# Performance work log

Measured on AMD Instinct MI355X. Metric: run time of the kernel, lower is better.

## Reference

```python
import jax, jax.numpy as jnp
import numpy as np

D_MODEL = 1024
H = 16
D_HEAD = D_MODEL // H
EPS = 1e-5  # torch LayerNorm default


def setup_inputs() -> dict:
    key = jax.random.key(0)
    ks = jax.random.split(key, 10)
    bs, seq = 4, 2048
    scale = 1.0 / np.sqrt(D_MODEL)
    return {
        "q": jax.random.normal(ks[0], (bs, seq, D_MODEL), jnp.float32),
        "k": jax.random.normal(ks[1], (bs, seq, D_MODEL), jnp.float32),
        "v": jax.random.normal(ks[2], (bs, seq, D_MODEL), jnp.float32),
        "zero_mask": jnp.zeros((bs, 1, 1, seq), jnp.float32),
        "Wq": jax.random.normal(ks[3], (D_MODEL, D_MODEL), jnp.float32) * scale,
        "Wk": jax.random.normal(ks[4], (D_MODEL, D_MODEL), jnp.float32) * scale,
        "Wv": jax.random.normal(ks[5], (D_MODEL, D_MODEL), jnp.float32) * scale,
        "Wo": jax.random.normal(ks[6], (D_MODEL, D_MODEL), jnp.float32) * scale,
        "gamma": jnp.ones((D_MODEL,), jnp.float32),
        "beta": jnp.zeros((D_MODEL,), jnp.float32),
    }


def reference(q, k, v, zero_mask, Wq, Wk, Wv, Wo, gamma, beta):
    bs, seq_q, _ = q.shape
    seq_k = k.shape[1]
    residual = q
    # Projections (torch Linear: x @ W.T), split into heads -> (bs, h, seq, d)
    qh = (q @ Wq.T).reshape(bs, seq_q, H, D_HEAD).transpose(0, 2, 1, 3)
    kh = (k @ Wk.T).reshape(bs, seq_k, H, D_HEAD).transpose(0, 2, 1, 3)
    vh = (v @ Wv.T).reshape(bs, seq_k, H, D_HEAD).transpose(0, 2, 1, 3)
    # Scaled dot-product attention with additive -1e9 * zero_mask
    att = jnp.einsum("bhqd,bhkd->bhqk", qh, kh) / np.sqrt(D_HEAD)
    att = att + zero_mask * -1e9
    att = jax.nn.softmax(att, axis=-1)
    # dropout: identity in eval-mode reference
    ctx = jnp.einsum("bhqk,bhkd->bhqd", att, vh)
    ctx = ctx.transpose(0, 2, 1, 3).reshape(bs, seq_q, D_MODEL)
    out = ctx @ Wo.T
    out = out + residual
    # LayerNorm over last dim
    mu = jnp.mean(out, axis=-1, keepdims=True)
    var = jnp.var(out, axis=-1, keepdims=True)
    out = (out - mu) * jax.lax.rsqrt(var + EPS) * gamma + beta
    return out
```

## Files before the change

kernel.cpp:

```cpp
#include <hip/hip_runtime.h>

typedef __bf16 bf16x8 __attribute__((ext_vector_type(8)));
typedef float  f32x4  __attribute__((ext_vector_type(4)));
typedef short  s16x4  __attribute__((ext_vector_type(4)));

#define D_MODEL 1024
#define SEQ 2048
#define BS 4
#define NH 16
#define DH 64
#define MTOT (BS * SEQ)

#define AS1 __attribute__((address_space(1)))
#define AS3 __attribute__((address_space(3)))

template <typename T>
__device__ inline bf16x8 ld8(const T* p);

template <>
__device__ inline bf16x8 ld8<float>(const float* p) {
    f32x4 a = *(const f32x4*)p;
    f32x4 b = *(const f32x4*)(p + 4);
    bf16x8 r;
    r[0] = (__bf16)a[0]; r[1] = (__bf16)a[1]; r[2] = (__bf16)a[2]; r[3] = (__bf16)a[3];
    r[4] = (__bf16)b[0]; r[5] = (__bf16)b[1]; r[6] = (__bf16)b[2]; r[7] = (__bf16)b[3];
    return r;
}

template <>
__device__ inline bf16x8 ld8<__bf16>(const __bf16* p) {
    return *(const bf16x8*)p;
}

__global__ __launch_bounds__(256) void cvt3_kernel(
    const float* __restrict__ a, const float* __restrict__ b, const float* __restrict__ c,
    __bf16* __restrict__ x, __bf16* __restrict__ y, __bf16* __restrict__ z)
{
    const float* s = (blockIdx.y == 0) ? a : (blockIdx.y == 1) ? b : c;
    __bf16*      d = (blockIdx.y == 0) ? x : (blockIdx.y == 1) ? y : z;
    const long i = ((long)blockIdx.x * 256 + threadIdx.x) * 8;
    *(bf16x8*)(d + i) = ld8<float>(s + i);
}

__global__ __launch_bounds__(256) void cvt4_kernel(
    const float* __restrict__ a, const float* __restrict__ b,
    const float* __restrict__ c, const float* __restrict__ e,
    __bf16* __restrict__ x, __bf16* __restrict__ y,
    __bf16* __restrict__ z, __bf16* __restrict__ w)
{
    const float* s = (blockIdx.y == 0) ? a : (blockIdx.y == 1) ? b : (blockIdx.y == 2) ? c : e;
    __bf16*      d = (blockIdx.y == 0) ? x : (blockIdx.y == 1) ? y : (blockIdx.y == 2) ? z : w;
    const long i = ((long)blockIdx.x * 256 + threadIdx.x) * 8;
    *(bf16x8*)(d + i) = ld8<float>(s + i);
}

__global__ __launch_bounds__(256) void gemm_bb(
    const __bf16* __restrict__ A, const __bf16* __restrict__ B,
    __bf16* __restrict__ C, int M, int N, int K)
{
    __shared__ __align__(16) __bf16 As[128 * 32];
    __shared__ __align__(16) __bf16 Bs[128 * 32];
    const int t = threadIdx.x;
    const int wave = t >> 6, lane = t & 63;
    const int quad = lane >> 4, l15 = lane & 15;
    const int wm = (wave >> 1) * 64, wn = (wave & 1) * 64;
    const long m0 = (long)blockIdx.x * 128;
    const long n0 = (long)blockIdx.y * 128;

    const __bf16* gA = A + (m0 + (t >> 2)) * (long)K + (t & 3) * 8;
    const __bf16* gB = B + (n0 + (t >> 2)) * (long)K + (t & 3) * 8;
    __bf16* lA0 = As + wave * 512;
    __bf16* lA1 = As + 2048 + wave * 512;
    __bf16* lB0 = Bs + wave * 512;
    __bf16* lB1 = Bs + 2048 + wave * 512;

    f32x4 acc[4][4] = {};

    for (int k0 = 0; k0 < K; k0 += 32) {
        __builtin_amdgcn_global_load_lds((const AS1 void*)(gA + k0),          (AS3 void*)lA0, 16, 0, 0);
        __builtin_amdgcn_global_load_lds((const AS1 void*)(gA + 64 * K + k0), (AS3 void*)lA1, 16, 0, 0);
        __builtin_amdgcn_global_load_lds((const AS1 void*)(gB + k0),          (AS3 void*)lB0, 16, 0, 0);
        __builtin_amdgcn_global_load_lds((const AS1 void*)(gB + 64 * K + k0), (AS3 void*)lB1, 16, 0, 0);
        __syncthreads();
        bf16x8 af[4], bfr[4];
#pragma unroll
        for (int i = 0; i < 4; ++i) af[i]  = *(const bf16x8*)&As[(wm + i * 16 + l15) * 32 + quad * 8];
#pragma unroll
        for (int i = 0; i < 4; ++i) bfr[i] = *(const bf16x8*)&Bs[(wn + i * 16 + l15) * 32 + quad * 8];
#pragma unroll
        for (int i = 0; i < 4; ++i)
#pragma unroll
            for (int j = 0; j < 4; ++j)
                acc[i][j] = __builtin_amdgcn_mfma_f32_16x16x32_bf16(af[i], bfr[j], acc[i][j], 0, 0, 0);
        __syncthreads();
    }

#pragma unroll
    for (int i = 0; i < 4; ++i)
#pragma unroll
        for (int j = 0; j < 4; ++j) {
            const long r = m0 + wm + i * 16 + quad * 4;
            const long c = n0 + wn + j * 16 + l15;
#pragma unroll
            for (int reg = 0; reg < 4; ++reg)
                C[(r + reg) * N + c] = (__bf16)acc[i][j][reg];
        }
}

template <typename TA, typename TB>
__global__ __launch_bounds__(256) void gemm_bt(
    const TA* __restrict__ A, const TB* __restrict__ B,
    __bf16* __restrict__ C, int M, int N, int K)
{
    __shared__ __align__(16) __bf16 As[128][48];
    __shared__ __align__(16) __bf16 Bs[128][48];
    const int t = threadIdx.x;
    const int wave = t >> 6, lane = t & 63;
    const int quad = lane >> 4, l15 = lane & 15;
    const int wm = (wave >> 1) * 64, wn = (wave & 1) * 64;
    const long m0 = (long)blockIdx.x * 128;
    const long n0 = (long)blockIdx.y * 128;
    const int sr = t >> 2;
    const int sc = (t & 3) * 8;

    f32x4 acc[4][4] = {};

    for (int k0 = 0; k0 < K; k0 += 32) {
        *(bf16x8*)&As[sr][sc]      = ld8<TA>(&A[(m0 + sr) * K + k0 + sc]);
        *(bf16x8*)&As[sr + 64][sc] = ld8<TA>(&A[(m0 + sr + 64) * K + k0 + sc]);
        *(bf16x8*)&Bs[sr][sc]      = ld8<TB>(&B[(n0 + sr) * K + k0 + sc]);
        *(bf16x8*)&Bs[sr + 64][sc] = ld8<TB>(&B[(n0 + sr + 64) * K + k0 + sc]);
        __syncthreads();
        bf16x8 af[4], bfr[4];
#pragma unroll
        for (int i = 0; i < 4; ++i) af[i]  = *(const bf16x8*)&As[wm + i * 16 + l15][quad * 8];
#pragma unroll
        for (int i = 0; i < 4; ++i) bfr[i] = *(const bf16x8*)&Bs[wn + i * 16 + l15][quad * 8];
#pragma unroll
        for (int i = 0; i < 4; ++i)
#pragma unroll
            for (int j = 0; j < 4; ++j)
                acc[i][j] = __builtin_amdgcn_mfma_f32_16x16x32_bf16(af[i], bfr[j], acc[i][j], 0, 0, 0);
        __syncthreads();
    }

#pragma unroll
    for (int i = 0; i < 4; ++i)
#pragma unroll
        for (int j = 0; j < 4; ++j) {
            const long r = m0 + wm + i * 16 + quad * 4;
            const long c = n0 + wn + j * 16 + l15;
#pragma unroll
            for (int reg = 0; reg < 4; ++reg)
                C[(r + reg) * N + c] = (__bf16)acc[i][j][reg];
        }
}

__global__ __launch_bounds__(256) void attn_kernel(
    const __bf16* Qp, const __bf16* __restrict__ Kp, const __bf16* __restrict__ Vp,
    const float* __restrict__ mask, __bf16* Ctx)
{
    __shared__ __align__(16) __bf16 Ks[64][72];
    __shared__ __align__(16) __bf16 Vt[64][76];
    __shared__ __align__(16) float  Ms[64];

    const int t = threadIdx.x;
    const int wave = t >> 6, lane = t & 63;
    const int quad = lane >> 4, l15 = lane & 15;
    const int qt = blockIdx.x;
    const int bh = blockIdx.y;
    const int b = bh >> 4, h = bh & 15;
    const long rowbase = (long)b * SEQ;
    const int q0 = qt * 128 + wave * 16;

    bf16x8 aq[2][2];
#pragma unroll
    for (int qi = 0; qi < 2; ++qi) {
        const long qrow = rowbase + q0 + qi * 64 + l15;
        const __bf16* qptr = Qp + qrow * D_MODEL + h * DH + quad * 8;
        aq[qi][0] = *(const bf16x8*)(qptr);
        aq[qi][1] = *(const bf16x8*)(qptr + 32);
    }

    float l_acc[2] = {0.f, 0.f};
    f32x4 acc_o[2][4] = {};

    const int sr = t >> 2, sc = (t & 3) * 16;
    const int kp2 = (t >> 3) * 2, dc = (t & 7) * 8;

    for (int kt = 0; kt < SEQ / 64; ++kt) {
        __syncthreads();
        {
            const __bf16* kptr = Kp + (rowbase + kt * 64 + sr) * D_MODEL + h * DH + sc;
            *(bf16x8*)&Ks[sr][sc]     = *(const bf16x8*)(kptr);
            *(bf16x8*)&Ks[sr][sc + 8] = *(const bf16x8*)(kptr + 8);
            const __bf16* vptr = Vp + (rowbase + kt * 64 + kp2) * D_MODEL + h * DH + dc;
            bf16x8 v0 = *(const bf16x8*)(vptr);
            bf16x8 v1 = *(const bf16x8*)(vptr + D_MODEL);
#pragma unroll
            for (int e = 0; e < 8; ++e) {
                union { __bf16 h2[2]; unsigned u; } pk;
                pk.h2[0] = v0[e]; pk.h2[1] = v1[e];
                *(unsigned*)&Vt[dc + e][kp2] = pk.u;
            }
            if (t < 64) Ms[t] = mask[(long)b * SEQ + kt * 64 + t] * -1e9f;
        }
        __syncthreads();

        bf16x8 kf[4][2];
#pragma unroll
        for (int nt = 0; nt < 4; ++nt)
#pragma unroll
            for (int ks = 0; ks < 2; ++ks)
                kf[nt][ks] = *(const bf16x8*)&Ks[nt * 16 + l15][ks * 32 + quad * 8];
        s16x4 vtf[4][4];
#pragma unroll
        for (int nt = 0; nt < 4; ++nt)
#pragma unroll
            for (int dt = 0; dt < 4; ++dt)
                vtf[nt][dt] = *(const s16x4*)&Vt[dt * 16 + l15][nt * 16 + quad * 4];
        f32x4 mv[4];
#pragma unroll
        for (int nt = 0; nt < 4; ++nt)
            mv[nt] = *(const f32x4*)&Ms[nt * 16 + quad * 4];

#pragma unroll
        for (int qi = 0; qi < 2; ++qi) {
            f32x4 st[4] = {};
#pragma unroll
            for (int ks = 0; ks < 2; ++ks)
#pragma unroll
                for (int nt = 0; nt < 4; ++nt)
                    st[nt] = __builtin_amdgcn_mfma_f32_16x16x32_bf16(kf[nt][ks], aq[qi][ks], st[nt], 0, 0, 0);
            s16x4 pp[4];
#pragma unroll
            for (int nt = 0; nt < 4; ++nt) {
                union { __bf16 hh[4]; s16x4 s; } u;
#pragma unroll
                for (int reg = 0; reg < 4; ++reg) {
                    const float pv = __expf(fmaf(st[nt][reg], 0.125f, mv[nt][reg]));
                    l_acc[qi] += pv;
                    u.hh[reg] = (__bf16)pv;
                }
                pp[nt] = u.s;
            }
#pragma unroll
            for (int nt = 0; nt < 4; ++nt)
#pragma unroll
                for (int dt = 0; dt < 4; ++dt)
                    acc_o[qi][dt] = __builtin_amdgcn_mfma_f32_16x16x16bf16_1k(pp[nt], vtf[nt][dt], acc_o[qi][dt], 0, 0, 0);
        }
    }

#pragma unroll
    for (int qi = 0; qi < 2; ++qi) {
        float l = l_acc[qi];
        l += __shfl_xor(l, 16, 64);
        l += __shfl_xor(l, 32, 64);
        const float inv = 1.f / l;
        float invq[4];
#pragma unroll
        for (int reg = 0; reg < 4; ++reg)
            invq[reg] = __shfl(inv, quad * 4 + reg, 64);
#pragma unroll
        for (int dt = 0; dt < 4; ++dt)
#pragma unroll
            for (int reg = 0; reg < 4; ++reg) {
                const long row = rowbase + q0 + qi * 64 + quad * 4 + reg;
                Ctx[row * D_MODEL + h * DH + dt * 16 + l15] = (__bf16)(acc_o[qi][dt][reg] * invq[reg]);
            }
    }
}

__global__ __launch_bounds__(256) void ln_kernel(
    const __bf16* __restrict__ Y, const float* __restrict__ R,
    const float* __restrict__ gamma, const float* __restrict__ beta,
    float* __restrict__ Out)
{
    __shared__ float red[8];
    const long row = blockIdx.x;
    const int t = threadIdx.x;
    const int wave = t >> 6, lane = t & 63;
    float x[4];
    float s = 0.f, s2 = 0.f;
#pragma unroll
    for (int i = 0; i < 4; ++i) {
        const int idx = i * 256 + t;
        const float v = (float)Y[row * D_MODEL + idx] + R[row * D_MODEL + idx];
        x[i] = v; s += v; s2 += v * v;
    }
#pragma unroll
    for (int off = 32; off >= 1; off >>= 1) {
        s  += __shfl_xor(s, off, 64);
        s2 += __shfl_xor(s2, off, 64);
    }
    if (lane == 0) { red[wave] = s; red[4 + wave] = s2; }
    __syncthreads();
    s  = red[0] + red[1] + red[2] + red[3];
    s2 = red[4] + red[5] + red[6] + red[7];
    const float mu   = s * (1.f / 1024.f);
    const float var  = s2 * (1.f / 1024.f) - mu * mu;
    const float rstd = rsqrtf(var + 1e-5f);
#pragma unroll
    for (int i = 0; i < 4; ++i) {
        const int idx = i * 256 + t;
        Out[row * D_MODEL + idx] = (x[i] - mu) * rstd * gamma[idx] + beta[idx];
    }
}

extern "C" void kernel_launch(void* const* d_in, const int* in_sizes, int n_in,
                              void* d_out, int out_size, void* d_ws, size_t ws_size,
                              hipStream_t stream)
{
    const float* q     = (const float*)d_in[0];
    const float* k     = (const float*)d_in[1];
    const float* v     = (const float*)d_in[2];
    const float* mask  = (const float*)d_in[3];
    const float* Wq    = (const float*)d_in[4];
    const float* Wk    = (const float*)d_in[5];
    const float* Wv    = (const float*)d_in[6];
    const float* Wo    = (const float*)d_in[7];
    const float* gamma = (const float*)d_in[8];
    const float* beta  = (const float*)d_in[9];
    float* out = (float*)d_out;

    const long NACT = (long)MTOT * D_MODEL;
    const long NW   = (long)D_MODEL * D_MODEL;
    dim3 gg(MTOT / 128, D_MODEL / 128);
    dim3 ga(SEQ / 128, BS * NH);

    if (ws_size >= (size_t)NACT * 2 * 4) {
        __bf16* qb = (__bf16*)d_ws;
        __bf16* kb = qb + NACT;
        __bf16* vb = kb + NACT;
        __bf16* Kp = vb + NACT;
        __bf16* Vp = (__bf16*)d_out;
        __bf16* Wb = Vp + NACT;
        __bf16 *Wqb = Wb, *Wkb = Wb + NW, *Wvb = Wb + 2 * NW, *Wob = Wb + 3 * NW;
        __bf16* Qp = kb;
        __bf16* Y  = qb;

        cvt3_kernel<<<dim3(NACT / 2048, 3), 256, 0, stream>>>(q, k, v, qb, kb, vb);
        cvt4_kernel<<<dim3(NW / 2048, 4), 256, 0, stream>>>(Wq, Wk, Wv, Wo, Wqb, Wkb, Wvb, Wob);

        gemm_bb<<<gg, 256, 0, stream>>>(kb, Wkb, Kp, MTOT, D_MODEL, D_MODEL);
        gemm_bb<<<gg, 256, 0, stream>>>(qb, Wqb, Qp, MTOT, D_MODEL, D_MODEL);
        gemm_bb<<<gg, 256, 0, stream>>>(vb, Wvb, Vp, MTOT, D_MODEL, D_MODEL);

        attn_kernel<<<ga, 256, 0, stream>>>(Qp, Kp, Vp, mask, Qp);

        gemm_bb<<<gg, 256, 0, stream>>>(Qp, Wob, Y, MTOT, D_MODEL, D_MODEL);
        ln_kernel<<<MTOT, 256, 0, stream>>>(Y, q, gamma, beta, out);
    } else {
        __bf16* Qp = (__bf16*)d_ws;
        __bf16* Kp = Qp + NACT;
        __bf16* Vp = (__bf16*)d_out;
        __bf16* Y  = Kp;

        gemm_bt<float, float><<<gg, 256, 0, stream>>>(q, Wq, Qp, MTOT, D_MODEL, D_MODEL);
        gemm_bt<float, float><<<gg, 256, 0, stream>>>(k, Wk, Kp, MTOT, D_MODEL, D_MODEL);
        gemm_bt<float, float><<<gg, 256, 0, stream>>>(v, Wv, Vp, MTOT, D_MODEL, D_MODEL);

        attn_kernel<<<ga, 256, 0, stream>>>(Qp, Kp, Vp, mask, Qp);

        gemm_bt<__bf16, float><<<gg, 256, 0, stream>>>(Qp, Wo, Y, MTOT, D_MODEL, D_MODEL);
        ln_kernel<<<MTOT, 256, 0, stream>>>(Y, q, gamma, beta, out);
    }
}
```

Baseline: 412.2 us.

## Fuse QKV projections with in-kernel fp32 conversion and widen attention tiles

Removes the separate activation conversion pass and merges the three QKV projection GEMMs into one launch over a z-dimension. That launch converts fp32 activations to bf16 while loading, and streams the bf16 weights through global_load_lds. The attention kernel now covers 256 queries per block instead of 128, so each K/V tile is reused across twice as many queries. It preloads the whole scaled mask row into LDS once and uses exp2 with prefolded log2e constants. The trade-offs are more registers per thread in attention, fewer attention blocks, and dropping the fallback path for small workspaces.

After: 412.1 us. About the same (-0.0%).

```diff
diff --git a/kernel.cpp b/kernel.cpp
--- a/kernel.cpp
+++ b/kernel.cpp
@@ -32,16 +32,6 @@
     return *(const bf16x8*)p;
 }
 
-__global__ __launch_bounds__(256) void cvt3_kernel(
-    const float* __restrict__ a, const float* __restrict__ b, const float* __restrict__ c,
-    __bf16* __restrict__ x, __bf16* __restrict__ y, __bf16* __restrict__ z)
-{
-    const float* s = (blockIdx.y == 0) ? a : (blockIdx.y == 1) ? b : c;
-    __bf16*      d = (blockIdx.y == 0) ? x : (blockIdx.y == 1) ? y : z;
-    const long i = ((long)blockIdx.x * 256 + threadIdx.x) * 8;
-    *(bf16x8*)(d + i) = ld8<float>(s + i);
-}
-
 __global__ __launch_bounds__(256) void cvt4_kernel(
     const float* __restrict__ a, const float* __restrict__ b,
     const float* __restrict__ c, const float* __restrict__ e,
@@ -52,6 +42,64 @@
     __bf16*      d = (blockIdx.y == 0) ? x : (blockIdx.y == 1) ? y : (blockIdx.y == 2) ? z : w;
     const long i = ((long)blockIdx.x * 256 + threadIdx.x) * 8;
     *(bf16x8*)(d + i) = ld8<float>(s + i);
+}
+
+__global__ __launch_bounds__(256) void gemm_qkv(
+    const float* __restrict__ q, const float* __restrict__ k, const float* __restrict__ v,
+    const __bf16* __restrict__ Wb,
+    __bf16* __restrict__ Qp, __bf16* __restrict__ Kp, __bf16* __restrict__ Vp)
+{
+    __shared__ __align__(16) __bf16 As[128][48];
+    __shared__ __align__(16) __bf16 Bs[128 * 32];
+    const int K = D_MODEL, N = D_MODEL;
+    const int z = blockIdx.z;
+    const float* A = (z == 0) ? q : (z == 1) ? k : v;
+    const __bf16* B = Wb + (long)z * D_MODEL * D_MODEL;
+    __bf16* C = (z == 0) ? Qp : (z == 1) ? Kp : Vp;
+
+    const int t = threadIdx.x;
+    const int wave = t >> 6, lane = t & 63;
+    const int quad = lane >> 4, l15 = lane & 15;
+    const int wm = (wave >> 1) * 64, wn = (wave & 1) * 64;
+    const long m0 = (long)blockIdx.x * 128;
+    const long n0 = (long)blockIdx.y * 128;
+    const int sr = t >> 2, sc = (t & 3) * 8;
+
+    const __bf16* gB = B + (n0 + (t >> 2)) * (long)K + (t & 3) * 8;
+    __bf16* lB0 = Bs + wave * 512;
+    __bf16* lB1 = Bs + 2048 + wave * 512;
+
+    f32x4 acc[4][4] = {};
+
+    for (int k0 = 0; k0 < K; k0 += 32) {
+        __builtin_amdgcn_global_load_lds((const AS1 void*)(gB + k0),          (AS3 void*)lB0, 16, 0, 0);
+        __builtin_amdgcn_global_load_lds((const AS1 void*)(gB + 64 * K + k0), (AS3 void*)lB1, 16, 0, 0);
+        *(bf16x8*)&As[sr][sc]      = ld8<float>(&A[(m0 + sr) * K + k0 + sc]);
+        *(bf16x8*)&As[sr + 64][sc] = ld8<float>(&A[(m0 + sr + 64) * K + k0 + sc]);
+        __syncthreads();
+        bf16x8 af[4], bfr[4];
+#pragma unroll
+        for (int i = 0; i < 4; ++i) af[i]  = *(const bf16x8*)&As[wm + i * 16 + l15][quad * 8];
+#pragma unroll
+        for (int i = 0; i < 4; ++i) bfr[i] = *(const bf16x8*)&Bs[(wn + i * 16 + l15) * 32 + quad * 8];
+#pragma unroll
+        for (int i = 0; i < 4; ++i)
+#pragma unroll
+            for (int j = 0; j < 4; ++j)
+                acc[i][j] = __builtin_amdgcn_mfma_f32_16x16x32_bf16(af[i], bfr[j], acc[i][j], 0, 0, 0);
+        __syncthreads();
+    }
+
+#pragma unroll
+    for (int i = 0; i < 4; ++i)
+#pragma unroll
+        for (int j = 0; j < 4; ++j) {
+            const long r = m0 + wm + i * 16 + quad * 4;
+            const long c = n0 + wn + j * 16 + l15;
+#pragma unroll
+            for (int reg = 0; reg < 4; ++reg)
+                C[(r + reg) * N + c] = (__bf16)acc[i][j][reg];
+        }
 }
 
 __global__ __launch_bounds__(256) void gemm_bb(
@@ -107,62 +155,13 @@
         }
 }
 
-template <typename TA, typename TB>
-__global__ __launch_bounds__(256) void gemm_bt(
-    const TA* __restrict__ A, const TB* __restrict__ B,
-    __bf16* __restrict__ C, int M, int N, int K)
-{
-    __shared__ __align__(16) __bf16 As[128][48];
-    __shared__ __align__(16) __bf16 Bs[128][48];
-    const int t = threadIdx.x;
-    const int wave = t >> 6, lane = t & 63;
-    const int quad = lane >> 4, l15 = lane & 15;
-    const int wm = (wave >> 1) * 64, wn = (wave & 1) * 64;
-    const long m0 = (long)blockIdx.x * 128;
-    const long n0 = (long)blockIdx.y * 128;
-    const int sr = t >> 2;
-    const int sc = (t & 3) * 8;
-
-    f32x4 acc[4][4] = {};
-
-    for (int k0 = 0; k0 < K; k0 += 32) {
-        *(bf16x8*)&As[sr][sc]      = ld8<TA>(&A[(m0 + sr) * K + k0 + sc]);
-        *(bf16x8*)&As[sr + 64][sc] = ld8<TA>(&A[(m0 + sr + 64) * K + k0 + sc]);
-        *(bf16x8*)&Bs[sr][sc]      = ld8<TB>(&B[(n0 + sr) * K + k0 + sc]);
-        *(bf16x8*)&Bs[sr + 64][sc] = ld8<TB>(&B[(n0 + sr + 64) * K + k0 + sc]);
-        __syncthreads();
-        bf16x8 af[4], bfr[4];
-#pragma unroll
-        for (int i = 0; i < 4; ++i) af[i]  = *(const bf16x8*)&As[wm + i * 16 + l15][quad * 8];
-#pragma unroll
-        for (int i = 0; i < 4; ++i) bfr[i] = *(const bf16x8*)&Bs[wn + i * 16 + l15][quad * 8];
-#pragma unroll
-        for (int i = 0; i < 4; ++i)
-#pragma unroll
-            for (int j = 0; j < 4; ++j)
-                acc[i][j] = __builtin_amdgcn_mfma_f32_16x16x32_bf16(af[i], bfr[j], acc[i][j], 0, 0, 0);
-        __syncthreads();
-    }
-
-#pragma unroll
-    for (int i = 0; i < 4; ++i)
-#pragma unroll
-        for (int j = 0; j < 4; ++j) {
-            const long r = m0 + wm + i * 16 + quad * 4;
-            const long c = n0 + wn + j * 16 + l15;
-#pragma unroll
-            for (int reg = 0; reg < 4; ++reg)
-                C[(r + reg) * N + c] = (__bf16)acc[i][j][reg];
-        }
-}
-
-__global__ __launch_bounds__(256) void attn_kernel(
+__global__ __launch_bounds__(256, 2) void attn_kernel(
     const __bf16* Qp, const __bf16* __restrict__ Kp, const __bf16* __restrict__ Vp,
     const float* __restrict__ mask, __bf16* Ctx)
 {
     __shared__ __align__(16) __bf16 Ks[64][72];
     __shared__ __align__(16) __bf16 Vt[64][76];
-    __shared__ __align__(16) float  Ms[64];
+    __shared__ __align__(16) float  Msk[SEQ];
 
     const int t = threadIdx.x;
     const int wave = t >> 6, lane = t & 63;
@@ -171,22 +170,34 @@
     const int bh = blockIdx.y;
     const int b = bh >> 4, h = bh & 15;
     const long rowbase = (long)b * SEQ;
-    const int q0 = qt * 128 + wave * 16;
-
-    bf16x8 aq[2][2];
-#pragma unroll
-    for (int qi = 0; qi < 2; ++qi) {
+    const int q0 = qt * 256 + wave * 16;
+
+    {
+        const float C2 = -1e9f * 1.44269504f;
+        f32x4 m0 = *(const f32x4*)&mask[rowbase + t * 8];
+        f32x4 m1 = *(const f32x4*)&mask[rowbase + t * 8 + 4];
+        f32x4 s0, s1;
+#pragma unroll
+        for (int e = 0; e < 4; ++e) { s0[e] = m0[e] * C2; s1[e] = m1[e] * C2; }
+        *(f32x4*)&Msk[t * 8]     = s0;
+        *(f32x4*)&Msk[t * 8 + 4] = s1;
+    }
+
+    bf16x8 aq[4][2];
+#pragma unroll
+    for (int qi = 0; qi < 4; ++qi) {
         const long qrow = rowbase + q0 + qi * 64 + l15;
         const __bf16* qptr = Qp + qrow * D_MODEL + h * DH + quad * 8;
         aq[qi][0] = *(const bf16x8*)(qptr);
         aq[qi][1] = *(const bf16x8*)(qptr + 32);
     }
 
-    float l_acc[2] = {0.f, 0.f};
-    f32x4 acc_o[2][4] = {};
+    float l_acc[4] = {};
+    f32x4 acc_o[4][4] = {};
 
     const int sr = t >> 2, sc = (t & 3) * 16;
     const int kp2 = (t >> 3) * 2, dc = (t & 7) * 8;
+    const float C1 = 0.125f * 1.44269504f;
 
     for (int kt = 0; kt < SEQ / 64; ++kt) {
         __syncthreads();
@@ -203,7 +214,6 @@
                 pk.h2[0] = v0[e]; pk.h2[1] = v1[e];
                 *(unsigned*)&Vt[dc + e][kp2] = pk.u;
             }
-            if (t < 64) Ms[t] = mask[(long)b * SEQ + kt * 64 + t] * -1e9f;
         }
         __syncthreads();
 
@@ -222,10 +232,10 @@
         f32x4 mv[4];
 #pragma unroll
         for (int nt = 0; nt < 4; ++nt)
-            mv[nt] = *(const f32x4*)&Ms[nt * 16 + quad * 4];
-
-#pragma unroll
-        for (int qi = 0; qi < 2; ++qi) {
+            mv[nt] = *(const f32x4*)&Msk[kt * 64 + nt * 16 + quad * 4];
+
+#pragma unroll
+        for (int qi = 0; qi < 4; ++qi) {
             f32x4 st[4] = {};
 #pragma unroll
             for (int ks = 0; ks < 2; ++ks)
@@ -238,7 +248,7 @@
                 union { __bf16 hh[4]; s16x4 s; } u;
 #pragma unroll
                 for (int reg = 0; reg < 4; ++reg) {
-                    const float pv = __expf(fmaf(st[nt][reg], 0.125f, mv[nt][reg]));
+                    const float pv = exp2f(fmaf(st[nt][reg], C1, mv[nt][reg]));
                     l_acc[qi] += pv;
                     u.hh[reg] = (__bf16)pv;
                 }
@@ -253,7 +263,7 @@
     }
 
 #pragma unroll
-    for (int qi = 0; qi < 2; ++qi) {
+    for (int qi = 0; qi < 4; ++qi) {
         float l = l_acc[qi];
         l += __shfl_xor(l, 16, 64);
         l += __shfl_xor(l, 32, 64);
@@ -326,44 +336,21 @@
 
     const long NACT = (long)MTOT * D_MODEL;
     const long NW   = (long)D_MODEL * D_MODEL;
-    dim3 gg(MTOT / 128, D_MODEL / 128);
-    dim3 ga(SEQ / 128, BS * NH);
-
-    if (ws_size >= (size_t)NACT * 2 * 4) {
-        __bf16* qb = (__bf16*)d_ws;
-        __bf16* kb = qb + NACT;
-        __bf16* vb = kb + NACT;
-        __bf16* Kp = vb + NACT;
-        __bf16* Vp = (__bf16*)d_out;
-        __bf16* Wb = Vp + NACT;
-        __bf16 *Wqb = Wb, *Wkb = Wb + NW, *Wvb = Wb + 2 * NW, *Wob = Wb + 3 * NW;
-        __bf16* Qp = kb;
-        __bf16* Y  = qb;
-
-        cvt3_kernel<<<dim3(NACT / 2048, 3), 256, 0, stream>>>(q, k, v, qb, kb, vb);
-        cvt4_kernel<<<dim3(NW / 2048, 4), 256, 0, stream>>>(Wq, Wk, Wv, Wo, Wqb, Wkb, Wvb, Wob);
-
-        gemm_bb<<<gg, 256, 0, stream>>>(kb, Wkb, Kp, MTOT, D_MODEL, D_MODEL);
-        gemm_bb<<<gg, 256, 0, stream>>>(qb, Wqb, Qp, MTOT, D_MODEL, D_MODEL);
-        gemm_bb<<<gg, 256, 0, stream>>>(vb, Wvb, Vp, MTOT, D_MODEL, D_MODEL);
-
-        attn_kernel<<<ga, 256, 0, stream>>>(Qp, Kp, Vp, mask, Qp);
-
-        gemm_bb<<<gg, 256, 0, stream>>>(Qp, Wob, Y, MTOT, D_MODEL, D_MODEL);
-        ln_kernel<<<MTOT, 256, 0, stream>>>(Y, q, gamma, beta, out);
-    } else {
-        __bf16* Qp = (__bf16*)d_ws;
-        __bf16* Kp = Qp + NACT;
-        __bf16* Vp = (__bf16*)d_out;
-        __bf16* Y  = Kp;
-
-        gemm_bt<float, float><<<gg, 256, 0, stream>>>(q, Wq, Qp, MTOT, D_MODEL, D_MODEL);
-        gemm_bt<float, float><<<gg, 256, 0, stream>>>(k, Wk, Kp, MTOT, D_MODEL, D_MODEL);
-        gemm_bt<float, float><<<gg, 256, 0, stream>>>(v, Wv, Vp, MTOT, D_MODEL, D_MODEL);
-
-        attn_kernel<<<ga, 256, 0, stream>>>(Qp, Kp, Vp, mask, Qp);
-
-        gemm_bt<__bf16, float><<<gg, 256, 0, stream>>>(Qp, Wo, Y, MTOT, D_MODEL, D_MODEL);
-        ln_kernel<<<MTOT, 256, 0, stream>>>(Y, q, gamma, beta, out);
-    }
-}
+
+    __bf16* Qp = (__bf16*)d_ws;
+    __bf16* Kp = Qp + NACT;
+    __bf16* Vp = (__bf16*)d_out;
+    __bf16* Wb = Vp + NACT;
+    __bf16 *Wqb = Wb, *Wkb = Wb + NW, *Wvb = Wb + 2 * NW, *Wob = Wb + 3 * NW;
+    __bf16* Y = Kp;
+
+    cvt4_kernel<<<dim3(NW / 2048, 4), 256, 0, stream>>>(Wq, Wk, Wv, Wo, Wqb, Wkb, Wvb, Wob);
+
+    gemm_qkv<<<dim3(MTOT / 128, D_MODEL / 128, 3), 256, 0, stream>>>(q, k, v, Wqb, Qp, Kp, Vp);
+
+    attn_kernel<<<dim3(SEQ / 256, BS * NH), 256, 0, stream>>>(Qp, Kp, Vp, mask, Qp);
+
+    gemm_bb<<<dim3(MTOT / 128, D_MODEL / 128), 256, 0, stream>>>(Qp, Wob, Y, MTOT, D_MODEL, D_MODEL);
+
+    ln_kernel<<<MTOT, 256, 0, stream>>>(Y, q, gamma, beta, out);
+}
```
